# Kernel tuning notes

Hardware: AMD Instinct MI355X
Metric: run time of the kernel (lower is better)

## Reference

```python
import jax, jax.numpy as jnp
import numpy as np

N = 4096   # support size
B = 512    # number of histograms (columns)


def setup_inputs() -> dict:
    key = jax.random.key(0)
    kU, kP, kK = jax.random.split(key, 3)
    # u must satisfy u < lamda; uniform [0,1) with lamda=10 is safe.
    U = jax.random.uniform(kU, (N, B), dtype=jnp.float32)
    # strictly positive histograms (avoid log(0))
    P = jax.random.uniform(kP, (N, B), dtype=jnp.float32) + 0.01
    # positive Gibbs kernel
    K = jax.random.uniform(kK, (N, N), dtype=jnp.float32) + 1e-3
    return {"U": U, "P": P, "K": K, "eps": 1, "lamda": 10}


def reference(U, P, K, eps, lamda):
    """Vectorized OTModel.OT_unbal: sum over columns of the primal unbalanced OT
    value reconstructed from dual potential U.  gamma_ij = a_i * K_ij * f_j is
    never materialized; all reductions over gamma are contracted analytically.
    """
    eps = jnp.float32(eps)
    lamda = jnp.float32(lamda)
    # f in log domain: (lamda/eps) * log(lamda/(lamda-u))          [N, B]
    flog = (lamda / eps) * jnp.log(lamda / (lamda - U))
    f = jnp.exp(flog)
    # alpha/eps with the mean-scale stabilization from get_alpha_unbal
    scale = flog.mean(axis=0)                                      # [B]
    KF_stab = K @ jnp.exp(flog - scale)                            # [N, B]
    alpha_over_eps = jnp.log(P) - (jnp.log(KF_stab) + scale)       # [N, B]
    a = jnp.exp(alpha_over_eps)                                    # exp(alpha/eps)
    Kf = K @ f                                                     # [N, B]
    # (gamma @ flog).sum() = sum_i a_i * (K @ (f * flog))_i
    term1 = jnp.sum(a * (K @ (f * flog)))
    # (gamma.T @ (alpha/eps)).sum() = sum_i a_i * (alpha/eps)_i * (K @ f)_i
    term2 = jnp.sum(a * alpha_over_eps * Kf)
    # gamma.sum()
    term3 = jnp.sum(a * Kf)
    # gamma.sum(0)_j = f_j * (K^T @ a)_j
    gcol = f * (K.T @ a)                                           # [N, B]
    # q from get_q_unbal (unstabilized, as in the original)
    q = (lamda / (lamda - U)) ** (lamda / eps + 1.0) * (K.T @ (P / Kf))
    # KL(a,b) = sum(a*log(a/b) - a)   (inputs strictly positive here)
    kl = jnp.sum(gcol * jnp.log(gcol / q) - gcol)
    return eps * (term1 + term2 - term3) + lamda * kl
```

## Files before the change

kernel.cpp:

```cpp
#include <hip/hip_runtime.h>

#define NN 4096
#define BB 512

typedef __attribute__((ext_vector_type(4))) float f32x4;
typedef __attribute__((ext_vector_type(16))) float f32x16;
typedef __attribute__((ext_vector_type(4))) int i32x4;
typedef __attribute__((ext_vector_type(8))) int i32x8;
typedef unsigned short ushort;
typedef unsigned char uchar;
typedef unsigned int uint;
typedef __attribute__((ext_vector_type(4))) ushort ushort4v;

#define ASCALE 16384.0f
#define AINV   6.103515625e-05f
#define SCL1   0x7f7f7f7f

__device__ __forceinline__ float scal_val(const void* p) {
    int b = *(const int*)p;
    if (b >= 1 && b <= 1000000) return (float)b;
    return __int_as_float(b);
}

__device__ __forceinline__ ushort f2bf(float x) {
    unsigned u = __float_as_uint(x);
    u += 0x7fffu + ((u >> 16) & 1u);
    return (ushort)(u >> 16);
}
__device__ __forceinline__ float bf2f(ushort b) {
    return __uint_as_float((uint)b << 16);
}

__device__ __forceinline__ uint pack4_fp8(float a, float b, float c, float d) {
    int v = __builtin_amdgcn_cvt_pk_fp8_f32(a, b, 0, false);
    v = __builtin_amdgcn_cvt_pk_fp8_f32(c, d, v, true);
    return (uint)v;
}

__device__ __forceinline__ void gload16(const void* g, void* l) {
    __builtin_amdgcn_global_load_lds(
        (const __attribute__((address_space(1))) unsigned int*)g,
        (__attribute__((address_space(3))) unsigned int*)l, 16, 0, 0);
}

__device__ __forceinline__ double wave_sum(double v) {
#pragma unroll
    for (int s = 32; s > 0; s >>= 1) v += __shfl_down(v, s, 64);
    return v;
}

__device__ __forceinline__ int offA(int i, int k) {
    return (((i >> 7) * 64 + (k >> 6)) << 13) + ((i & 127) << 6) +
           ((((k >> 4) & 3) ^ ((i >> 1) & 3)) << 4) + (k & 15);
}
__device__ __forceinline__ int offB(int j, int k) {
    return (((j >> 6) * 64 + (k >> 6)) << 12) + ((j & 63) << 6) +
           ((((k >> 4) & 3) ^ ((j >> 1) & 3)) << 4) + (k & 15);
}

__device__ __forceinline__ i32x8 frag64(const uchar* rowbase, int u0byte) {
    i32x4 lo = *(const i32x4*)(rowbase + u0byte);
    i32x4 hi = *(const i32x4*)(rowbase + (u0byte ^ 16));
    i32x8 r;
    r[0] = lo[0]; r[1] = lo[1]; r[2] = lo[2]; r[3] = lo[3];
    r[4] = hi[0]; r[5] = hi[1]; r[6] = hi[2]; r[7] = hi[3];
    return r;
}


__global__ __launch_bounds__(256) void k_prep(const float* __restrict__ K,
                                              const float* __restrict__ U,
                                              uchar* __restrict__ Kb,
                                              uchar* __restrict__ KTb,
                                              uchar* __restrict__ fT,
                                              const void* epsp, const void* lamp) {
    __shared__ float tile[64][65];
    const int t = threadIdx.x;
    const int tx = t & 15, ty = t >> 4;
    const int bid = blockIdx.x;

    if (bid < 4096) {
        const int c0 = (bid & 63) * 64, r0 = (bid >> 6) * 64;
#pragma unroll
        for (int it = 0; it < 4; ++it) {
            int row = ty + it * 16;
            int i = r0 + row;
            float4 v = *(const float4*)&K[(size_t)i * NN + c0 + tx * 4];
            *(uint*)&Kb[offA(i, c0 + tx * 4)] = pack4_fp8(v.x, v.y, v.z, v.w);
            tile[row][tx * 4 + 0] = v.x;
            tile[row][tx * 4 + 1] = v.y;
            tile[row][tx * 4 + 2] = v.z;
            tile[row][tx * 4 + 3] = v.w;
        }
        __syncthreads();
#pragma unroll
        for (int it = 0; it < 4; ++it) {
            int row = ty + it * 16;
            int i = c0 + row;
            int k = r0 + tx * 4;
            *(uint*)&KTb[offA(i, k)] =
                pack4_fp8(tile[tx * 4 + 0][row], tile[tx * 4 + 1][row],
                          tile[tx * 4 + 2][row], tile[tx * 4 + 3][row]);
        }
    } else {
        const int r = bid - 4096;
        const int c0 = (r & 7) * 64;
        const int r0 = (r >> 3) * 64;
        const float eps = scal_val(epsp), lam = scal_val(lamp);
        const float rr = lam / eps;
#pragma unroll
        for (int it = 0; it < 4; ++it) {
            int row = ty + it * 16;
            float4 v = *(const float4*)&U[(size_t)(r0 + row) * BB + c0 + tx * 4];
            float uu[4] = {v.x, v.y, v.z, v.w};
#pragma unroll
            for (int k = 0; k < 4; ++k) {
                float L = __logf(lam / (lam - uu[k]));
                tile[row][tx * 4 + k] = __expf(rr * L);
            }
        }
        __syncthreads();
#pragma unroll
        for (int it = 0; it < 4; ++it) {
            int row = ty + it * 16;
            int j = c0 + row;
            int k = r0 + tx * 4;
            *(uint*)&fT[offB(j, k)] =
                pack4_fp8(tile[tx * 4 + 0][row], tile[tx * 4 + 1][row],
                          tile[tx * 4 + 2][row], tile[tx * 4 + 3][row]);
        }
    }
}

__global__ __launch_bounds__(256) void k_gemm1(const uchar* __restrict__ Kb,
                                               const uchar* __restrict__ fT,
                                               ushort* __restrict__ Y1b) {
    __shared__ __align__(16) uchar As[3][128 * 64];
    __shared__ __align__(16) uchar Bf[3][64 * 64];

    const int tid = threadIdx.x;
    const int lane = tid & 63;
    const int w = tid >> 6;
    const int bid = blockIdx.x;
    const int kh = bid & 3;
    const int i0 = ((bid >> 2) & 31) * 128;
    const int j0 = (bid >> 7) * 64;
    const int h = lane >> 5;
    const int r = lane & 31;
    const int u0b = (((h << 1) ^ ((r >> 1) & 3)) << 4);

    f32x16 acc0 = {}, acc1 = {};

    const uchar* apanel = Kb + ((size_t)(i0 >> 7) << 19);
    const uchar* bpanel = fT + ((size_t)(j0 >> 6) << 18);

    auto stage = [&](int ks, int b) {
        const uchar* ga = apanel + ((size_t)ks << 13) + w * 2048 + lane * 16;
        gload16(ga, &As[b][w * 2048]);
        gload16(ga + 1024, &As[b][w * 2048 + 1024]);
        const uchar* gb = bpanel + ((size_t)ks << 12) + w * 1024 + lane * 16;
        gload16(gb, &Bf[b][w * 1024]);
    };

    const int ks0 = kh * 16;
    stage(ks0, 0);
    stage(ks0 + 1, 1);
    int cur = 0, pf = 2;
    for (int step = 0; step < 16; ++step) {
        if (step < 15) asm volatile("s_waitcnt vmcnt(3)" ::: "memory");
        else           asm volatile("s_waitcnt vmcnt(0)" ::: "memory");
        __builtin_amdgcn_s_barrier();
        __builtin_amdgcn_sched_barrier(0);
        if (step < 14) stage(ks0 + step + 2, pf);
        i32x8 av = frag64(&As[cur][(w * 32 + r) << 6], u0b);
        i32x8 bv0 = frag64(&Bf[cur][r << 6], u0b);
        i32x8 bv1 = frag64(&Bf[cur][(32 + r) << 6], u0b);
        acc0 = __builtin_amdgcn_mfma_scale_f32_32x32x64_f8f6f4(
            av, bv0, acc0, 0, 0, 0, SCL1, 0, SCL1);
        acc1 = __builtin_amdgcn_mfma_scale_f32_32x32x64_f8f6f4(
            av, bv1, acc1, 0, 0, 0, SCL1, 0, SCL1);
        __builtin_amdgcn_sched_barrier(0);
        cur = (cur == 2) ? 0 : cur + 1;
        pf = (pf == 2) ? 0 : pf + 1;
    }

    ushort* o1 = Y1b + (size_t)kh * NN * BB;
#pragma unroll
    for (int reg = 0; reg < 16; ++reg) {
        const int row = i0 + w * 32 + (reg & 3) + 8 * (reg >> 2) + 4 * h;
        o1[(size_t)row * BB + j0 + r] = f2bf(acc0[reg]);
        o1[(size_t)row * BB + j0 + 32 + r] = f2bf(acc1[reg]);
    }
}

__global__ __launch_bounds__(256) void k_epi(const ushort* __restrict__ Y1b,
                                             const float* __restrict__ P,
                                             uchar* __restrict__ aT,
                                             double* __restrict__ parts) {
    __shared__ float ta[64][65];
    __shared__ double bred[4][2];
    const int t = threadIdx.x;
    const int lane = t & 63;
    const int w = t >> 6;
    const int tx = t & 15, ty = t >> 4;
    const int j0 = blockIdx.x * 64;
    const int i0 = blockIdx.y * 64;
    const int bid = blockIdx.y * 8 + blockIdx.x;
    const size_t H = (size_t)NN * BB;

    double t2 = 0.0, t3 = 0.0;
#pragma unroll
    for (int it = 0; it < 4; ++it) {
        int row = ty + it * 16;
        size_t off = (size_t)(i0 + row) * BB + j0 + tx * 4;
        ushort4v q0 = *(const ushort4v*)(Y1b + off);
        ushort4v q1 = *(const ushort4v*)(Y1b + H + off);
        ushort4v q2 = *(const ushort4v*)(Y1b + 2 * H + off);
        ushort4v q3 = *(const ushort4v*)(Y1b + 3 * H + off);
        float4 p4 = *(const float4*)(P + off);
        float pv[4] = {p4.x, p4.y, p4.z, p4.w};
#pragma unroll
        for (int e = 0; e < 4; ++e) {
            float y1 = bf2f(q0[e]) + bf2f(q1[e]) + bf2f(q2[e]) + bf2f(q3[e]);
            float aij = pv[e] / y1;
            t2 += (double)(pv[e] * __logf(aij));
            t3 += (double)pv[e];
            ta[row][tx * 4 + e] = aij * ASCALE;
        }
    }
    __syncthreads();
#pragma unroll
    for (int it = 0; it < 4; ++it) {
        int row = ty + it * 16;
        int j = j0 + row;
        *(uint*)&aT[offB(j, i0 + tx * 4)] =
            pack4_fp8(ta[tx * 4 + 0][row], ta[tx * 4 + 1][row],
                      ta[tx * 4 + 2][row], ta[tx * 4 + 3][row]);
    }

    t2 = wave_sum(t2); t3 = wave_sum(t3);
    if (lane == 0) { bred[w][0] = t2; bred[w][1] = t3; }
    __syncthreads();
    if (t == 0) {
        double b = 0, c = 0;
#pragma unroll
        for (int ww = 0; ww < 4; ++ww) { b += bred[ww][0]; c += bred[ww][1]; }
        parts[2048 + bid] = b;
        parts[2560 + bid] = c;
    }
}

__global__ __launch_bounds__(256) void k_gemm2(const uchar* __restrict__ KTb,
                                               const uchar* __restrict__ aT,
                                               const float* __restrict__ U,
                                               const void* epsp, const void* lamp,
                                               double* __restrict__ parts) {
    __shared__ __align__(16) uchar As[3][128 * 64];
    __shared__ __align__(16) uchar Bs[3][64 * 64];
    __shared__ double bred[4][2];

    const float eps = scal_val(epsp), lam = scal_val(lamp);
    const float rr = lam / eps;
    const int tid = threadIdx.x;
    const int lane = tid & 63;
    const int w = tid >> 6;
    const int bid = blockIdx.x;
    const int kh = bid & 3;
    const int i0 = ((bid >> 2) & 31) * 128;
    const int j0 = (bid >> 7) * 64;
    const int h = lane >> 5;
    const int r = lane & 31;
    const int u0b = (((h << 1) ^ ((r >> 1) & 3)) << 4);

    f32x16 acc0 = {}, acc1 = {};

    const uchar* apanel = KTb + ((size_t)(i0 >> 7) << 19);
    const uchar* bpanel = aT + ((size_t)(j0 >> 6) << 18);

    auto stage = [&](int ks, int b) {
        const uchar* ga = apanel + ((size_t)ks << 13) + w * 2048 + lane * 16;
        gload16(ga, &As[b][w * 2048]);
        gload16(ga + 1024, &As[b][w * 2048 + 1024]);
        const uchar* gb = bpanel + ((size_t)ks << 12) + w * 1024 + lane * 16;
        gload16(gb, &Bs[b][w * 1024]);
    };

    const int ks0 = kh * 16;
    stage(ks0, 0);
    stage(ks0 + 1, 1);
    int cur = 0, pf = 2;
    for (int step = 0; step < 16; ++step) {
        if (step < 15) asm volatile("s_waitcnt vmcnt(3)" ::: "memory");
        else           asm volatile("s_waitcnt vmcnt(0)" ::: "memory");
        __builtin_amdgcn_s_barrier();
        __builtin_amdgcn_sched_barrier(0);
        if (step < 14) stage(ks0 + step + 2, pf);
        i32x8 av = frag64(&As[cur][(w * 32 + r) << 6], u0b);
        i32x8 bv0 = frag64(&Bs[cur][r << 6], u0b);
        i32x8 bv1 = frag64(&Bs[cur][(32 + r) << 6], u0b);
        acc0 = __builtin_amdgcn_mfma_scale_f32_32x32x64_f8f6f4(
            av, bv0, acc0, 0, 0, 0, SCL1, 0, SCL1);
        acc1 = __builtin_amdgcn_mfma_scale_f32_32x32x64_f8f6f4(
            av, bv1, acc1, 0, 0, 0, SCL1, 0, SCL1);
        __builtin_amdgcn_sched_barrier(0);
        cur = (cur == 2) ? 0 : cur + 1;
        pf = (pf == 2) ? 0 : pf + 1;
    }

    double t1p = 0.0, klp = 0.0;
#pragma unroll
    for (int reg = 0; reg < 16; ++reg) {
        const int ib = i0 + w * 32 + (reg & 3) + 8 * (reg >> 2) + 4 * h;
#pragma unroll
        for (int nt = 0; nt < 2; ++nt) {
            const int j = j0 + nt * 32 + r;
            float s = (nt ? acc1[reg] : acc0[reg]) * AINV;
            float u = U[(size_t)ib * BB + j];
            float L = __logf(lam / (lam - u));
            float fv = __expf(rr * L);
            t1p += (double)(fv * rr * L * s);
            klp -= (double)(fv * (1.0f + L) * s);
        }
    }

    t1p = wave_sum(t1p); klp = wave_sum(klp);
    if (lane == 0) { bred[w][0] = t1p; bred[w][1] = klp; }
    __syncthreads();
    if (tid == 0) {
        double a = 0, b = 0;
#pragma unroll
        for (int ww = 0; ww < 4; ++ww) { a += bred[ww][0]; b += bred[ww][1]; }
        parts[bid] = a;
        parts[1024 + bid] = b;
    }
}

__global__ __launch_bounds__(256) void k_final(const double* __restrict__ parts,
                                               const void* epsp, const void* lamp,
                                               float* __restrict__ out) {
    __shared__ double red[4][4];
    const int tid = threadIdx.x;
    const int lane = tid & 63, w = tid >> 6;
    double s0 = 0.0, s1 = 0.0, s2 = 0.0, s3 = 0.0;
    for (int i = tid; i < 1024; i += 256) {
        s0 += parts[i];
        s1 += parts[1024 + i];
    }
    for (int i = tid; i < 512; i += 256) {
        s2 += parts[2048 + i];
        s3 += parts[2560 + i];
    }
    s0 = wave_sum(s0); s1 = wave_sum(s1); s2 = wave_sum(s2); s3 = wave_sum(s3);
    if (lane == 0) { red[w][0] = s0; red[w][1] = s1; red[w][2] = s2; red[w][3] = s3; }
    __syncthreads();
    if (tid == 0) {
        double t1 = 0, kl = 0, t2 = 0, t3 = 0;
#pragma unroll
        for (int ww = 0; ww < 4; ++ww) {
            t1 += red[ww][0]; kl += red[ww][1]; t2 += red[ww][2]; t3 += red[ww][3];
        }
        float eps = scal_val(epsp), lam = scal_val(lamp);
        out[0] = (float)((double)eps * (t1 + t2 - t3) + (double)lam * kl);
    }
}

extern "C" void kernel_launch(void* const* d_in, const int* in_sizes, int n_in,
                              void* d_out, int out_size, void* d_ws, size_t ws_size,
                              hipStream_t stream) {
    const float* U = (const float*)d_in[0];
    const float* P = (const float*)d_in[1];
    const float* K = (const float*)d_in[2];
    const void* epsp = d_in[3];
    const void* lamp = d_in[4];

    double* parts = (double*)d_ws;
    char* base = (char*)d_ws + (64 << 10);
    uchar* Kb   = (uchar*)base;
    uchar* KTb  = (uchar*)(base + ((size_t)16 << 20));
    uchar* fT   = (uchar*)(base + ((size_t)32 << 20));
    uchar* aT   = (uchar*)(base + ((size_t)34 << 20));
    ushort* Y1b = (ushort*)(base + ((size_t)36 << 20));

    k_prep<<<4608, 256, 0, stream>>>(K, U, Kb, KTb, fT, epsp, lamp);
    k_gemm1<<<1024, 256, 0, stream>>>(Kb, fT, Y1b);
    k_epi<<<dim3(8, 64), 256, 0, stream>>>(Y1b, P, aT, parts);
    k_gemm2<<<1024, 256, 0, stream>>>(KTb, aT, U, epsp, lamp, parts);
    k_final<<<1, 256, 0, stream>>>(parts, epsp, lamp, (float*)d_out);
}
```

Baseline: 155.7 us.

## Enlarge GEMM tiles to 128x128 with 8 waves and fuse final reduction

Result: slower. 173.8 us (+11.7%).

```diff
diff --git a/kernel.cpp b/kernel.cpp
--- a/kernel.cpp
+++ b/kernel.cpp
@@ -73,11 +73,14 @@
                                               uchar* __restrict__ Kb,
                                               uchar* __restrict__ KTb,
                                               uchar* __restrict__ fT,
-                                              const void* epsp, const void* lamp) {
+                                              const void* epsp, const void* lamp,
+                                              double* __restrict__ parts) {
     __shared__ float tile[64][65];
     const int t = threadIdx.x;
     const int tx = t & 15, ty = t >> 4;
     const int bid = blockIdx.x;
+
+    if (bid == 0 && t == 0) *(unsigned int*)(parts + 3072) = 0u;
 
     if (bid < 4096) {
         const int c0 = (bid & 63) * 64, r0 = (bid >> 6) * 64;
@@ -132,19 +135,20 @@
     }
 }
 
-__global__ __launch_bounds__(256) void k_gemm1(const uchar* __restrict__ Kb,
+__global__ __launch_bounds__(512) void k_gemm1(const uchar* __restrict__ Kb,
                                                const uchar* __restrict__ fT,
                                                ushort* __restrict__ Y1b) {
     __shared__ __align__(16) uchar As[3][128 * 64];
-    __shared__ __align__(16) uchar Bf[3][64 * 64];
+    __shared__ __align__(16) uchar Bs[3][128 * 64];
 
     const int tid = threadIdx.x;
     const int lane = tid & 63;
     const int w = tid >> 6;
+    const int wm = w >> 2, wn = w & 3;
     const int bid = blockIdx.x;
     const int kh = bid & 3;
     const int i0 = ((bid >> 2) & 31) * 128;
-    const int j0 = (bid >> 7) * 64;
+    const int j0 = (bid >> 7) * 128;
     const int h = lane >> 5;
     const int r = lane & 31;
     const int u0b = (((h << 1) ^ ((r >> 1) & 3)) << 4);
@@ -155,11 +159,11 @@
     const uchar* bpanel = fT + ((size_t)(j0 >> 6) << 18);
 
     auto stage = [&](int ks, int b) {
-        const uchar* ga = apanel + ((size_t)ks << 13) + w * 2048 + lane * 16;
-        gload16(ga, &As[b][w * 2048]);
-        gload16(ga + 1024, &As[b][w * 2048 + 1024]);
-        const uchar* gb = bpanel + ((size_t)ks << 12) + w * 1024 + lane * 16;
-        gload16(gb, &Bf[b][w * 1024]);
+        const uchar* ga = apanel + ((size_t)ks << 13) + w * 1024 + lane * 16;
+        gload16(ga, &As[b][w * 1024]);
+        const uchar* gb = bpanel + (((size_t)(w >> 2)) << 18) +
+                          ((size_t)ks << 12) + (w & 3) * 1024 + lane * 16;
+        gload16(gb, &Bs[b][w * 1024]);
     };
 
     const int ks0 = kh * 16;
@@ -167,29 +171,32 @@
     stage(ks0 + 1, 1);
     int cur = 0, pf = 2;
     for (int step = 0; step < 16; ++step) {
-        if (step < 15) asm volatile("s_waitcnt vmcnt(3)" ::: "memory");
+        if (step < 15) asm volatile("s_waitcnt vmcnt(2)" ::: "memory");
         else           asm volatile("s_waitcnt vmcnt(0)" ::: "memory");
         __builtin_amdgcn_s_barrier();
         __builtin_amdgcn_sched_barrier(0);
         if (step < 14) stage(ks0 + step + 2, pf);
-        i32x8 av = frag64(&As[cur][(w * 32 + r) << 6], u0b);
-        i32x8 bv0 = frag64(&Bf[cur][r << 6], u0b);
-        i32x8 bv1 = frag64(&Bf[cur][(32 + r) << 6], u0b);
+        i32x8 av0 = frag64(&As[cur][(wm * 64 + r) << 6], u0b);
+        i32x8 av1 = frag64(&As[cur][(wm * 64 + 32 + r) << 6], u0b);
+        i32x8 bv = frag64(&Bs[cur][(wn * 32 + r) << 6], u0b);
+        __builtin_amdgcn_s_setprio(1);
         acc0 = __builtin_amdgcn_mfma_scale_f32_32x32x64_f8f6f4(
-            av, bv0, acc0, 0, 0, 0, SCL1, 0, SCL1);
+            av0, bv, acc0, 0, 0, 0, SCL1, 0, SCL1);
         acc1 = __builtin_amdgcn_mfma_scale_f32_32x32x64_f8f6f4(
-            av, bv1, acc1, 0, 0, 0, SCL1, 0, SCL1);
+            av1, bv, acc1, 0, 0, 0, SCL1, 0, SCL1);
+        __builtin_amdgcn_s_setprio(0);
         __builtin_amdgcn_sched_barrier(0);
         cur = (cur == 2) ? 0 : cur + 1;
         pf = (pf == 2) ? 0 : pf + 1;
     }
 
     ushort* o1 = Y1b + (size_t)kh * NN * BB;
+    const int jb = j0 + wn * 32 + r;
 #pragma unroll
     for (int reg = 0; reg < 16; ++reg) {
-        const int row = i0 + w * 32 + (reg & 3) + 8 * (reg >> 2) + 4 * h;
-        o1[(size_t)row * BB + j0 + r] = f2bf(acc0[reg]);
-        o1[(size_t)row * BB + j0 + 32 + r] = f2bf(acc1[reg]);
+        const int row = i0 + wm * 64 + (reg & 3) + 8 * (reg >> 2) + 4 * h;
+        o1[(size_t)row * BB + jb] = f2bf(acc0[reg]);
+        o1[(size_t)(row + 32) * BB + jb] = f2bf(acc1[reg]);
     }
 }
 
@@ -250,24 +257,27 @@
     }
 }
 
-__global__ __launch_bounds__(256) void k_gemm2(const uchar* __restrict__ KTb,
+__global__ __launch_bounds__(512) void k_gemm2(const uchar* __restrict__ KTb,
                                                const uchar* __restrict__ aT,
                                                const float* __restrict__ U,
                                                const void* epsp, const void* lamp,
-                                               double* __restrict__ parts) {
+                                               double* __restrict__ parts,
+                                               float* __restrict__ out) {
     __shared__ __align__(16) uchar As[3][128 * 64];
-    __shared__ __align__(16) uchar Bs[3][64 * 64];
-    __shared__ double bred[4][2];
+    __shared__ __align__(16) uchar Bs[3][128 * 64];
+    __shared__ double bred[8][4];
+    __shared__ int lastflag;
 
     const float eps = scal_val(epsp), lam = scal_val(lamp);
     const float rr = lam / eps;
     const int tid = threadIdx.x;
     const int lane = tid & 63;
     const int w = tid >> 6;
+    const int wm = w >> 2, wn = w & 3;
     const int bid = blockIdx.x;
     const int kh = bid & 3;
     const int i0 = ((bid >> 2) & 31) * 128;
-    const int j0 = (bid >> 7) * 64;
+    const int j0 = (bid >> 7) * 128;
     const int h = lane >> 5;
     const int r = lane & 31;
     const int u0b = (((h << 1) ^ ((r >> 1) & 3)) << 4);
@@ -278,10 +288,10 @@
     const uchar* bpanel = aT + ((size_t)(j0 >> 6) << 18);
 
     auto stage = [&](int ks, int b) {
-        const uchar* ga = apanel + ((size_t)ks << 13) + w * 2048 + lane * 16;
-        gload16(ga, &As[b][w * 2048]);
-        gload16(ga + 1024, &As[b][w * 2048 + 1024]);
-        const uchar* gb = bpanel + ((size_t)ks << 12) + w * 1024 + lane * 16;
+        const uchar* ga = apanel + ((size_t)ks << 13) + w * 1024 + lane * 16;
+        gload16(ga, &As[b][w * 1024]);
+        const uchar* gb = bpanel + (((size_t)(w >> 2)) << 18) +
+                          ((size_t)ks << 12) + (w & 3) * 1024 + lane * 16;
         gload16(gb, &Bs[b][w * 1024]);
     };
 
@@ -290,31 +300,34 @@
     stage(ks0 + 1, 1);
     int cur = 0, pf = 2;
     for (int step = 0; step < 16; ++step) {
-        if (step < 15) asm volatile("s_waitcnt vmcnt(3)" ::: "memory");
+        if (step < 15) asm volatile("s_waitcnt vmcnt(2)" ::: "memory");
         else           asm volatile("s_waitcnt vmcnt(0)" ::: "memory");
         __builtin_amdgcn_s_barrier();
         __builtin_amdgcn_sched_barrier(0);
         if (step < 14) stage(ks0 + step + 2, pf);
-        i32x8 av = frag64(&As[cur][(w * 32 + r) << 6], u0b);
-        i32x8 bv0 = frag64(&Bs[cur][r << 6], u0b);
-        i32x8 bv1 = frag64(&Bs[cur][(32 + r) << 6], u0b);
+        i32x8 av0 = frag64(&As[cur][(wm * 64 + r) << 6], u0b);
+        i32x8 av1 = frag64(&As[cur][(wm * 64 + 32 + r) << 6], u0b);
+        i32x8 bv = frag64(&Bs[cur][(wn * 32 + r) << 6], u0b);
+        __builtin_amdgcn_s_setprio(1);
         acc0 = __builtin_amdgcn_mfma_scale_f32_32x32x64_f8f6f4(
-            av, bv0, acc0, 0, 0, 0, SCL1, 0, SCL1);
+            av0, bv, acc0, 0, 0, 0, SCL1, 0, SCL1);
         acc1 = __builtin_amdgcn_mfma_scale_f32_32x32x64_f8f6f4(
-            av, bv1, acc1, 0, 0, 0, SCL1, 0, SCL1);
+            av1, bv, acc1, 0, 0, 0, SCL1, 0, SCL1);
+        __builtin_amdgcn_s_setprio(0);
         __builtin_amdgcn_sched_barrier(0);
         cur = (cur == 2) ? 0 : cur + 1;
         pf = (pf == 2) ? 0 : pf + 1;
     }
 
     double t1p = 0.0, klp = 0.0;
+    const int j = j0 + wn * 32 + r;
 #pragma unroll
     for (int reg = 0; reg < 16; ++reg) {
-        const int ib = i0 + w * 32 + (reg & 3) + 8 * (reg >> 2) + 4 * h;
-#pragma unroll
-        for (int nt = 0; nt < 2; ++nt) {
-            const int j = j0 + nt * 32 + r;
-            float s = (nt ? acc1[reg] : acc0[reg]) * AINV;
+        const int crow = (reg & 3) + 8 * (reg >> 2) + 4 * h;
+#pragma unroll
+        for (int mt = 0; mt < 2; ++mt) {
+            const int ib = i0 + wm * 64 + mt * 32 + crow;
+            float s = (mt ? acc1[reg] : acc0[reg]) * AINV;
             float u = U[(size_t)ib * BB + j];
             float L = __logf(lam / (lam - u));
             float fv = __expf(rr * L);
@@ -329,38 +342,37 @@
     if (tid == 0) {
         double a = 0, b = 0;
 #pragma unroll
-        for (int ww = 0; ww < 4; ++ww) { a += bred[ww][0]; b += bred[ww][1]; }
+        for (int ww = 0; ww < 8; ++ww) { a += bred[ww][0]; b += bred[ww][1]; }
         parts[bid] = a;
-        parts[1024 + bid] = b;
-    }
-}
-
-__global__ __launch_bounds__(256) void k_final(const double* __restrict__ parts,
-                                               const void* epsp, const void* lamp,
-                                               float* __restrict__ out) {
-    __shared__ double red[4][4];
-    const int tid = threadIdx.x;
-    const int lane = tid & 63, w = tid >> 6;
-    double s0 = 0.0, s1 = 0.0, s2 = 0.0, s3 = 0.0;
-    for (int i = tid; i < 1024; i += 256) {
-        s0 += parts[i];
-        s1 += parts[1024 + i];
-    }
-    for (int i = tid; i < 512; i += 256) {
-        s2 += parts[2048 + i];
-        s3 += parts[2560 + i];
-    }
-    s0 = wave_sum(s0); s1 = wave_sum(s1); s2 = wave_sum(s2); s3 = wave_sum(s3);
-    if (lane == 0) { red[w][0] = s0; red[w][1] = s1; red[w][2] = s2; red[w][3] = s3; }
+        parts[512 + bid] = b;
+        __threadfence();
+        uint old = atomicAdd((unsigned int*)(parts + 3072), 1u);
+        lastflag = (old == 511) ? 1 : 0;
+    }
     __syncthreads();
-    if (tid == 0) {
-        double t1 = 0, kl = 0, t2 = 0, t3 = 0;
-#pragma unroll
-        for (int ww = 0; ww < 4; ++ww) {
-            t1 += red[ww][0]; kl += red[ww][1]; t2 += red[ww][2]; t3 += red[ww][3];
-        }
-        float eps = scal_val(epsp), lam = scal_val(lamp);
-        out[0] = (float)((double)eps * (t1 + t2 - t3) + (double)lam * kl);
+
+    if (lastflag) {
+        __threadfence();
+        const volatile double* vp = parts;
+        double s0 = vp[tid];
+        double s1 = vp[512 + tid];
+        double s2 = vp[2048 + tid];
+        double s3 = vp[2560 + tid];
+        s0 = wave_sum(s0); s1 = wave_sum(s1);
+        s2 = wave_sum(s2); s3 = wave_sum(s3);
+        if (lane == 0) {
+            bred[w][0] = s0; bred[w][1] = s1; bred[w][2] = s2; bred[w][3] = s3;
+        }
+        __syncthreads();
+        if (tid == 0) {
+            double t1 = 0, kl = 0, t2 = 0, t3 = 0;
+#pragma unroll
+            for (int ww = 0; ww < 8; ++ww) {
+                t1 += bred[ww][0]; kl += bred[ww][1];
+                t2 += bred[ww][2]; t3 += bred[ww][3];
+            }
+            out[0] = (float)((double)eps * (t1 + t2 - t3) + (double)lam * kl);
+        }
     }
 }
 
@@ -381,9 +393,8 @@
     uchar* aT   = (uchar*)(base + ((size_t)34 << 20));
     ushort* Y1b = (ushort*)(base + ((size_t)36 << 20));
 
-    k_prep<<<4608, 256, 0, stream>>>(K, U, Kb, KTb, fT, epsp, lamp);
-    k_gemm1<<<1024, 256, 0, stream>>>(Kb, fT, Y1b);
+    k_prep<<<4608, 256, 0, stream>>>(K, U, Kb, KTb, fT, epsp, lamp, parts);
+    k_gemm1<<<512, 512, 0, stream>>>(Kb, fT, Y1b);
     k_epi<<<dim3(8, 64), 256, 0, stream>>>(Y1b, P, aT, parts);
-    k_gemm2<<<1024, 256, 0, stream>>>(KTb, aT, U, epsp, lamp, parts);
-    k_final<<<1, 256, 0, stream>>>(parts, epsp, lamp, (float*)d_out);
-}
+    k_gemm2<<<512, 512, 0, stream>>>(KTb, aT, U, epsp, lamp, parts, (float*)d_out);
+}
```
